# Kernel optimization log

Measured on AMD Instinct MI355X. Metric: run time of the kernel, lower is better.

## Reference

```python
import jax, jax.numpy as jnp
import numpy as np

HEAD_NUM = 12
HEAD_SIZE = 64
INPUT_DIM = 768
BATCH = 2
SEQ = 2048
NEG = 1e12


def setup_inputs() -> dict:
    key = jax.random.key(0)
    k1, k2, k3 = jax.random.split(key, 3)
    x = jax.random.normal(k1, (BATCH, SEQ, INPUT_DIM), dtype=jnp.float32)
    W = jax.random.normal(k2, (INPUT_DIM, HEAD_NUM * HEAD_SIZE * 2), dtype=jnp.float32) * 0.02
    b = jax.random.normal(k3, (HEAD_NUM * HEAD_SIZE * 2,), dtype=jnp.float32) * 0.02
    mask = jnp.ones((BATCH, SEQ), dtype=jnp.int32)
    return {"x": x, "W": W, "b": b, "mask": mask}


def _rope_tables(n, d, dtype):
    # SinusoidalPositionEmbedding(head_size, 'zero'): pos[..., 0::2]=sin, 1::2=cos
    pos = jnp.arange(n, dtype=dtype)
    freqs = jnp.power(10000.0, -2.0 * jnp.arange(d // 2, dtype=dtype) / d)
    ang = pos[:, None] * freqs[None, :]  # [n, d/2]
    # K.repeat_elements(pos[..., 1::2], 2, -1) -> each cos value repeated twice
    cos_pos = jnp.repeat(jnp.cos(ang), 2, axis=-1)  # [n, d]
    sin_pos = jnp.repeat(jnp.sin(ang), 2, axis=-1)  # [n, d]
    return cos_pos[None, :, None, :], sin_pos[None, :, None, :]  # [1,n,1,d]


def _rotate_half(t):
    # stack([-t[...,1::2], t[...,::2]], -1).reshape(t.shape)
    t2 = jnp.stack([-t[..., 1::2], t[..., 0::2]], axis=-1)
    return t2.reshape(t.shape)


def reference(x, W, b, mask):
    bsz, n, _ = x.shape
    proj = (x @ W + b).reshape(bsz, n, HEAD_NUM, 2 * HEAD_SIZE)  # [b,n,h,2d]
    qw, kw = proj[..., :HEAD_SIZE], proj[..., HEAD_SIZE:]
    cos_pos, sin_pos = _rope_tables(n, HEAD_SIZE, x.dtype)
    qw = qw * cos_pos + _rotate_half(qw) * sin_pos
    kw = kw * cos_pos + _rotate_half(kw) * sin_pos
    logits = jnp.einsum('bmhd,bnhd->bhmn', qw, kw)  # [b,h,m,n]
    m = mask.astype(logits.dtype)
    logits = logits - (1.0 - m[:, None, :, None]) * NEG  # mask query axis (dim 2)
    logits = logits - (1.0 - m[:, None, None, :]) * NEG  # mask key axis (dim 3)
    tri = jnp.triu(jnp.ones((n, n), dtype=logits.dtype))  # band_part(0,-1): keep m<=n
    logits = logits - (1.0 - tri) * NEG
    return logits / (HEAD_SIZE ** 0.5)
```

## Files before the change

### kernel.cpp

```cpp
#include <hip/hip_runtime.h>

#define SEQ    2048
#define IND    768
#define NPROJ  1536
#define BHN    24
#define NEGV   1000000000000.0f

typedef __attribute__((ext_vector_type(4))) float f32x4;
typedef __attribute__((ext_vector_type(8))) short s16x8;
typedef __attribute__((ext_vector_type(8))) unsigned short u16x8;
typedef __attribute__((ext_vector_type(4))) unsigned short u16x4;

__device__ __forceinline__ unsigned short f2bf(float f) {
  unsigned int u = __builtin_bit_cast(unsigned int, f);
  u += 0x7fffu + ((u >> 16) & 1u);
  return (unsigned short)(u >> 16);
}

__device__ __forceinline__ void nt_store4(float* p, f32x4 v) {
  __builtin_nontemporal_store(v, (f32x4*)p);
}

__device__ __forceinline__ void barrier_lgkm() {
  asm volatile("s_waitcnt lgkmcnt(0)" ::: "memory");
  __builtin_amdgcn_s_barrier();
}

#define GLOAD_LDS16(g, l)                                              \
  __builtin_amdgcn_global_load_lds(                                    \
      (const __attribute__((address_space(1))) void*)(g),              \
      (__attribute__((address_space(3))) void*)(l), 16, 0, 0)

__device__ __forceinline__ void stage128x64(const unsigned short* __restrict__ src,
                                            size_t stride, int4* lds, int tid) {
  const int w = tid >> 6, l = tid & 63;
#pragma unroll
  for (int i = 0; i < 4; ++i) {
    int gb = w * 256 + i * 64;
    int G = gb + l;
    int row = G >> 3, g = G & 7;
    int cb = g ^ (row & 7);
    GLOAD_LDS16(src + (size_t)row * stride + cb * 8, lds + gb);
  }
}

__device__ __forceinline__ void fill_tile(int fid, const int* __restrict__ mask,
                                          float* __restrict__ out, int tid) {
  int bh = fid / 120;
  int t = fid - bh * 120;
  int mt = 1;
  while (t >= mt) { t -= mt; ++mt; }
  int nt = t;
  int b = bh / 12;
  int m0 = mt * 128, n0 = nt * 128;
  const float scale = 0.125f;
#pragma unroll
  for (int it = 0; it < 16; ++it) {
    int id = it * 256 + tid;
    int row = id >> 5, c4 = id & 31;
    int gm = m0 + row;
    float rm = (float)mask[b * SEQ + gm];
    int gn0 = n0 + c4 * 4;
    f32x4 v;
#pragma unroll
    for (int q = 0; q < 4; ++q) {
      float cm = (float)mask[b * SEQ + gn0 + q];
      v[q] = -(NEGV * ((1.f - rm) + (1.f - cm) + 1.f)) * scale;
    }
    nt_store4(out + ((size_t)bh * SEQ + gm) * SEQ + gn0, v);
  }
}

__global__ __launch_bounds__(256) void k_prep(const float* __restrict__ x,
                                              const float* __restrict__ W,
                                              unsigned short* __restrict__ xb,
                                              unsigned short* __restrict__ Wt,
                                              float* __restrict__ cosT,
                                              float* __restrict__ sinT,
                                              const int* __restrict__ mask,
                                              float* __restrict__ out) {
  __shared__ float Ws[64][65];
  const int bid = blockIdx.x;
  const int tid = threadIdx.x;

  if (bid < 1536) {
    int i = (bid * 256 + tid) * 8;
    float4 a = *(const float4*)(x + i);
    float4 b = *(const float4*)(x + i + 4);
    u16x8 o;
    o[0] = f2bf(a.x); o[1] = f2bf(a.y); o[2] = f2bf(a.z); o[3] = f2bf(a.w);
    o[4] = f2bf(b.x); o[5] = f2bf(b.y); o[6] = f2bf(b.z); o[7] = f2bf(b.w);
    *(u16x8*)(xb + i) = o;
  } else if (bid < 1824) {
    int tb = bid - 1536;
    int nt = tb % 24, kt = tb / 24;
    int n0 = nt * 64, k0 = kt * 64;
    int cr = tid >> 4;
    int cc = (tid & 15) * 4;
#pragma unroll
    for (int it = 0; it < 4; ++it) {
      int kr = it * 16 + cr;
      float4 v = *(const float4*)(W + (size_t)(k0 + kr) * NPROJ + n0 + cc);
      Ws[kr][cc + 0] = v.x; Ws[kr][cc + 1] = v.y;
      Ws[kr][cc + 2] = v.z; Ws[kr][cc + 3] = v.w;
    }
    __syncthreads();
#pragma unroll
    for (int it = 0; it < 4; ++it) {
      int nl = it * 16 + cr;
      u16x4 o;
#pragma unroll
      for (int q = 0; q < 4; ++q) o[q] = f2bf(Ws[cc + q][nl]);
      *(u16x4*)(Wt + (size_t)(n0 + nl) * IND + k0 + cc) = o;
    }
  } else if (bid < 2080) {
    int i = (bid - 1824) * 256 + tid;
    int s = i >> 5, f = i & 31;
    float freq = exp2f(-(float)f * (13.287712379549449f / 32.0f));
    float ang = (float)s * freq;
    float sv, cv;
    sincosf(ang, &sv, &cv);
    cosT[i] = cv; sinT[i] = sv;
  } else {
    fill_tile(bid - 2080, mask, out, tid);
  }
}

__global__ __launch_bounds__(256, 2) void k_projfill(const unsigned short* __restrict__ xb,
                                                     const unsigned short* __restrict__ Wt,
                                                     const float* __restrict__ bias,
                                                     unsigned short* __restrict__ Qb,
                                                     unsigned short* __restrict__ Kb,
                                                     const float* __restrict__ cosT,
                                                     const float* __restrict__ sinT,
                                                     const int* __restrict__ mask,
                                                     float* __restrict__ out) {
  __shared__ int4 smem2[4096];
  const int tid = threadIdx.x;

  if (blockIdx.x >= 384) {
    fill_tile(512 + (int)blockIdx.x - 384, mask, out, tid);
    return;
  }

  int4* As4 = smem2;
  int4* Bs4 = smem2 + 2048;
  const int bidl = blockIdx.x;
  const int bid = (bidl & 7) * 48 + (bidl >> 3);
  const int nt = bid % 12, mt = bid / 12;
  const int m0 = mt * 128, n0 = nt * 128;
  const int wid = tid >> 6, lane = tid & 63;
  const int wr = wid >> 1, wc = wid & 1;
  const int lr = lane & 15, kg = lane >> 4;

  f32x4 acc[4][4] = {};

  const unsigned short* Abase = xb + (size_t)m0 * IND;
  const unsigned short* Bbase = Wt + (size_t)n0 * IND;

  stage128x64(Abase, IND, As4, tid);
  stage128x64(Bbase, IND, Bs4, tid);
  __syncthreads();

  for (int kt = 0; kt < 12; ++kt) {
    int cur = kt & 1;
    if (kt < 11) {
      stage128x64(Abase + (kt + 1) * 64, IND, As4 + (cur ^ 1) * 1024, tid);
      stage128x64(Bbase + (kt + 1) * 64, IND, Bs4 + (cur ^ 1) * 1024, tid);
    }
    const int4* Ac = As4 + cur * 1024;
    const int4* Bc = Bs4 + cur * 1024;
#pragma unroll
    for (int kk = 0; kk < 2; ++kk) {
      s16x8 af[4], bfr[4];
#pragma unroll
      for (int i = 0; i < 4; ++i) {
        int r = wr * 64 + i * 16 + lr;
        af[i] = *(const s16x8*)&Ac[r * 8 + ((kk * 4 + kg) ^ (r & 7))];
      }
#pragma unroll
      for (int j = 0; j < 4; ++j) {
        int r = wc * 64 + j * 16 + lr;
        bfr[j] = *(const s16x8*)&Bc[r * 8 + ((kk * 4 + kg) ^ (r & 7))];
      }
#pragma unroll
      for (int i = 0; i < 4; ++i)
#pragma unroll
        for (int j = 0; j < 4; ++j)
          acc[i][j] = __builtin_amdgcn_mfma_f32_16x16x32_bf16(af[i], bfr[j], acc[i][j], 0, 0, 0);
    }
    __syncthreads();
  }

  unsigned short* Cs = (unsigned short*)As4;
#pragma unroll
  for (int i = 0; i < 4; ++i) {
#pragma unroll
    for (int j = 0; j < 4; ++j) {
      int colr = wc * 64 + j * 16 + lr;
      int col = n0 + colr;
      float bcol = bias[col];
      int d = col & 63;
#pragma unroll
      for (int r = 0; r < 4; ++r) {
        int rowr = wr * 64 + i * 16 + kg * 4 + r;
        int s = (m0 + rowr) & (SEQ - 1);
        float v = acc[i][j][r] + bcol;
        float p = __shfl_xor(v, 1);
        int ti = s * 32 + (d >> 1);
        float cv = cosT[ti], sv = sinT[ti];
        float o = (col & 1) ? (v * cv + p * sv) : (v * cv - p * sv);
        int gs = (colr >> 3) ^ (rowr & 15);
        Cs[rowr * 128 + gs * 8 + (colr & 7)] = f2bf(o);
      }
    }
  }
  barrier_lgkm();
#pragma unroll
  for (int it = 0; it < 8; ++it) {
    int id = it * 256 + tid;
    int rowr = id >> 4, g = id & 15;
    int gs = g ^ (rowr & 15);
    u16x8 v = *(const u16x8*)&Cs[rowr * 128 + gs * 8];
    int m = m0 + rowr;
    int s = m & (SEQ - 1), bb = m >> 11;
    int colg = n0 + g * 8;
    int h = colg >> 7;
    int d0 = colg & 63;
    unsigned short* dst = ((colg & 64) == 0) ? Qb : Kb;
    *(u16x8*)(dst + ((size_t)(bb * 12 + h) * SEQ + s) * 64 + d0) = v;
  }
}

__global__ __launch_bounds__(256, 4) void k_attn(const unsigned short* __restrict__ Qb,
                                                 const unsigned short* __restrict__ Kb,
                                                 const int* __restrict__ mask,
                                                 float* __restrict__ out) {
  __shared__ int4 smem[2048];
  int4* Qs4 = smem;
  int4* Ks4 = smem + 1024;

  const int b0 = blockIdx.x;
  const int lin = (b0 & 7) * 408 + (b0 >> 3);
  int bh = lin / 136;
  int t = lin - bh * 136;
  int mt = 0;
  while (t >= 16 - mt) { t -= 16 - mt; ++mt; }
  const int nt = mt + t;
  const int b = bh / 12;
  const int tid = threadIdx.x;
  const int m0 = mt * 128, n0 = nt * 128;
  const float scale = 0.125f;

  const int wid = tid >> 6, lane = tid & 63;
  const int wr = wid >> 1, wc = wid & 1;
  const int lr = lane & 15, kg = lane >> 4;

  stage128x64(Qb + ((size_t)bh * SEQ + m0) * 64, 64, Qs4, tid);
  stage128x64(Kb + ((size_t)bh * SEQ + n0) * 64, 64, Ks4, tid);
  __syncthreads();

  f32x4 acc[4][4] = {};
#pragma unroll
  for (int kk = 0; kk < 2; ++kk) {
    s16x8 af[4], bfr[4];
#pragma unroll
    for (int i = 0; i < 4; ++i) {
      int r = wr * 64 + i * 16 + lr;
      af[i] = *(const s16x8*)&Qs4[r * 8 + ((kk * 4 + kg) ^ (r & 7))];
    }
#pragma unroll
    for (int j = 0; j < 4; ++j) {
      int r = wc * 64 + j * 16 + lr;
      bfr[j] = *(const s16x8*)&Ks4[r * 8 + ((kk * 4 + kg) ^ (r & 7))];
    }
#pragma unroll
    for (int i = 0; i < 4; ++i)
#pragma unroll
      for (int j = 0; j < 4; ++j)
        acc[i][j] = __builtin_amdgcn_mfma_f32_16x16x32_bf16(af[i], bfr[j], acc[i][j], 0, 0, 0);
  }

  barrier_lgkm();
  float* Cs = (float*)smem;

#pragma unroll
  for (int c = 0; c < 2; ++c) {
    if (wr == c) {
#pragma unroll
      for (int i = 0; i < 4; ++i)
#pragma unroll
        for (int j = 0; j < 4; ++j) {
          int col = wc * 64 + j * 16 + lr;
          int g = col >> 2;
#pragma unroll
          for (int r = 0; r < 4; ++r) {
            int rl = i * 16 + kg * 4 + r;
            int gs = g ^ (rl & 7);
            Cs[rl * 128 + gs * 4 + (col & 3)] = acc[i][j][r];
          }
        }
    }
    barrier_lgkm();
#pragma unroll
    for (int it = 0; it < 8; ++it) {
      int id = it * 256 + tid;
      int rl = id >> 5, g = id & 31;
      int gs = g ^ (rl & 7);
      f32x4 v = *(const f32x4*)&Cs[rl * 128 + gs * 4];
      int gm = m0 + c * 64 + rl;
      int gn0 = n0 + g * 4;
      float rmv = (float)mask[b * SEQ + gm];
      int4 cm = *(const int4*)&mask[b * SEQ + gn0];
      f32x4 o;
#pragma unroll
      for (int q = 0; q < 4; ++q) {
        int gn = gn0 + q;
        float cmv = (float)((const int*)&cm)[q];
        float pen = (1.f - rmv) + (1.f - cmv) + ((gn < gm) ? 1.f : 0.f);
        o[q] = (v[q] - NEGV * pen) * scale;
      }
      nt_store4(out + ((size_t)bh * SEQ + gm) * SEQ + gn0, o);
    }
    if (c == 0) barrier_lgkm();
  }
}

extern "C" void kernel_launch(void* const* d_in, const int* in_sizes, int n_in,
                              void* d_out, int out_size, void* d_ws, size_t ws_size,
                              hipStream_t stream) {
  const float* x    = (const float*)d_in[0];
  const float* W    = (const float*)d_in[1];
  const float* bias = (const float*)d_in[2];
  const int*   mask = (const int*)d_in[3];
  float* out = (float*)d_out;

  char* ws = (char*)d_ws;
  unsigned short* xb = (unsigned short*)(ws);
  unsigned short* Wt = (unsigned short*)(ws + 6291456);
  unsigned short* Qb = (unsigned short*)(ws + 6291456 + 2359296);
  unsigned short* Kb = (unsigned short*)(ws + 6291456 + 2359296 + 6291456);
  float* cosT = (float*)(ws + 6291456 + 2359296 + 6291456 + 6291456);
  float* sinT = (float*)(ws + 6291456 + 2359296 + 6291456 + 6291456 + 262144);

  k_prep<<<2592, 256, 0, stream>>>(x, W, xb, Wt, cosT, sinT, mask, out);
  k_projfill<<<2752, 256, 0, stream>>>(xb, Wt, bias, Qb, Kb, cosT, sinT, mask, out);
  k_attn<<<3264, 256, 0, stream>>>(Qb, Kb, mask, out);
}
```

Baseline: 94.97 us.

## Swap MFMA operand roles to store epilogues directly from registers, drop LDS staging

Both the projection GEMM and the attention-logits kernel swap the A/B operands of the MFMA so each lane's accumulator holds four consecutive output columns. The epilogues then apply bias, RoPE, masking and scaling in registers and write 8-byte (bf16) or 16-byte (fp32) vectors straight to global memory. This removes the LDS round trip and its barriers. In exchange, each wavefront's stores cover 16 rows with 64-byte segments per row instead of full contiguous rows, which may reduce write coalescing on the large fp32 output.

```diff
diff --git a/kernel.cpp b/kernel.cpp
--- a/kernel.cpp
+++ b/kernel.cpp
@@ -19,11 +19,6 @@
 
 __device__ __forceinline__ void nt_store4(float* p, f32x4 v) {
   __builtin_nontemporal_store(v, (f32x4*)p);
-}
-
-__device__ __forceinline__ void barrier_lgkm() {
-  asm volatile("s_waitcnt lgkmcnt(0)" ::: "memory");
-  __builtin_amdgcn_s_barrier();
 }
 
 #define GLOAD_LDS16(g, l)                                              \
@@ -175,13 +170,13 @@
       s16x8 af[4], bfr[4];
 #pragma unroll
       for (int i = 0; i < 4; ++i) {
-        int r = wr * 64 + i * 16 + lr;
-        af[i] = *(const s16x8*)&Ac[r * 8 + ((kk * 4 + kg) ^ (r & 7))];
+        int r = wc * 64 + i * 16 + lr;
+        af[i] = *(const s16x8*)&Bc[r * 8 + ((kk * 4 + kg) ^ (r & 7))];
       }
 #pragma unroll
       for (int j = 0; j < 4; ++j) {
-        int r = wc * 64 + j * 16 + lr;
-        bfr[j] = *(const s16x8*)&Bc[r * 8 + ((kk * 4 + kg) ^ (r & 7))];
+        int r = wr * 64 + j * 16 + lr;
+        bfr[j] = *(const s16x8*)&Ac[r * 8 + ((kk * 4 + kg) ^ (r & 7))];
       }
 #pragma unroll
       for (int i = 0; i < 4; ++i)
@@ -192,43 +187,28 @@
     __syncthreads();
   }
 
-  unsigned short* Cs = (unsigned short*)As4;
-#pragma unroll
-  for (int i = 0; i < 4; ++i) {
-#pragma unroll
-    for (int j = 0; j < 4; ++j) {
-      int colr = wc * 64 + j * 16 + lr;
-      int col = n0 + colr;
-      float bcol = bias[col];
-      int d = col & 63;
-#pragma unroll
-      for (int r = 0; r < 4; ++r) {
-        int rowr = wr * 64 + i * 16 + kg * 4 + r;
-        int s = (m0 + rowr) & (SEQ - 1);
-        float v = acc[i][j][r] + bcol;
-        float p = __shfl_xor(v, 1);
-        int ti = s * 32 + (d >> 1);
-        float cv = cosT[ti], sv = sinT[ti];
-        float o = (col & 1) ? (v * cv + p * sv) : (v * cv - p * sv);
-        int gs = (colr >> 3) ^ (rowr & 15);
-        Cs[rowr * 128 + gs * 8 + (colr & 7)] = f2bf(o);
-      }
-    }
-  }
-  barrier_lgkm();
-#pragma unroll
-  for (int it = 0; it < 8; ++it) {
-    int id = it * 256 + tid;
-    int rowr = id >> 4, g = id & 15;
-    int gs = g ^ (rowr & 15);
-    u16x8 v = *(const u16x8*)&Cs[rowr * 128 + gs * 8];
-    int m = m0 + rowr;
-    int s = m & (SEQ - 1), bb = m >> 11;
-    int colg = n0 + g * 8;
-    int h = colg >> 7;
-    int d0 = colg & 63;
-    unsigned short* dst = ((colg & 64) == 0) ? Qb : Kb;
-    *(u16x8*)(dst + ((size_t)(bb * 12 + h) * SEQ + s) * 64 + d0) = v;
+#pragma unroll
+  for (int j = 0; j < 4; ++j) {
+    int gm = m0 + wr * 64 + j * 16 + lr;
+    int s = gm & (SEQ - 1), bb = gm >> 11;
+#pragma unroll
+    for (int i = 0; i < 4; ++i) {
+      int col0 = n0 + wc * 64 + i * 16 + kg * 4;
+      int d0 = col0 & 63;
+      int h = col0 >> 7;
+      f32x4 bi = *(const f32x4*)&bias[col0];
+      int fi = s * 32 + (d0 >> 1);
+      float c0 = cosT[fi],     s0 = sinT[fi];
+      float c1 = cosT[fi + 1], s1 = sinT[fi + 1];
+      f32x4 v = acc[i][j] + bi;
+      u16x4 o;
+      o[0] = f2bf(v[0] * c0 - v[1] * s0);
+      o[1] = f2bf(v[1] * c0 + v[0] * s0);
+      o[2] = f2bf(v[2] * c1 - v[3] * s1);
+      o[3] = f2bf(v[3] * c1 + v[2] * s1);
+      unsigned short* dst = ((col0 & 64) == 0) ? Qb : Kb;
+      *(u16x4*)(dst + ((size_t)(bb * 12 + h) * SEQ + s) * 64 + d0) = o;
+    }
   }
 }
 
@@ -266,13 +246,13 @@
     s16x8 af[4], bfr[4];
 #pragma unroll
     for (int i = 0; i < 4; ++i) {
-      int r = wr * 64 + i * 16 + lr;
-      af[i] = *(const s16x8*)&Qs4[r * 8 + ((kk * 4 + kg) ^ (r & 7))];
+      int r = wc * 64 + i * 16 + lr;
+      af[i] = *(const s16x8*)&Ks4[r * 8 + ((kk * 4 + kg) ^ (r & 7))];
     }
 #pragma unroll
     for (int j = 0; j < 4; ++j) {
-      int r = wc * 64 + j * 16 + lr;
-      bfr[j] = *(const s16x8*)&Ks4[r * 8 + ((kk * 4 + kg) ^ (r & 7))];
+      int r = wr * 64 + j * 16 + lr;
+      bfr[j] = *(const s16x8*)&Qs4[r * 8 + ((kk * 4 + kg) ^ (r & 7))];
     }
 #pragma unroll
     for (int i = 0; i < 4; ++i)
@@ -281,37 +261,16 @@
         acc[i][j] = __builtin_amdgcn_mfma_f32_16x16x32_bf16(af[i], bfr[j], acc[i][j], 0, 0, 0);
   }
 
-  barrier_lgkm();
-  float* Cs = (float*)smem;
-
-#pragma unroll
-  for (int c = 0; c < 2; ++c) {
-    if (wr == c) {
-#pragma unroll
-      for (int i = 0; i < 4; ++i)
-#pragma unroll
-        for (int j = 0; j < 4; ++j) {
-          int col = wc * 64 + j * 16 + lr;
-          int g = col >> 2;
-#pragma unroll
-          for (int r = 0; r < 4; ++r) {
-            int rl = i * 16 + kg * 4 + r;
-            int gs = g ^ (rl & 7);
-            Cs[rl * 128 + gs * 4 + (col & 3)] = acc[i][j][r];
-          }
-        }
-    }
-    barrier_lgkm();
-#pragma unroll
-    for (int it = 0; it < 8; ++it) {
-      int id = it * 256 + tid;
-      int rl = id >> 5, g = id & 31;
-      int gs = g ^ (rl & 7);
-      f32x4 v = *(const f32x4*)&Cs[rl * 128 + gs * 4];
-      int gm = m0 + c * 64 + rl;
-      int gn0 = n0 + g * 4;
-      float rmv = (float)mask[b * SEQ + gm];
+#pragma unroll
+  for (int j = 0; j < 4; ++j) {
+    int gm = m0 + wr * 64 + j * 16 + lr;
+    float rmv = (float)mask[b * SEQ + gm];
+    float* orow = out + ((size_t)bh * SEQ + gm) * SEQ;
+#pragma unroll
+    for (int i = 0; i < 4; ++i) {
+      int gn0 = n0 + wc * 64 + i * 16 + kg * 4;
       int4 cm = *(const int4*)&mask[b * SEQ + gn0];
+      f32x4 v = acc[i][j];
       f32x4 o;
 #pragma unroll
       for (int q = 0; q < 4; ++q) {
@@ -320,9 +279,8 @@
         float pen = (1.f - rmv) + (1.f - cmv) + ((gn < gm) ? 1.f : 0.f);
         o[q] = (v[q] - NEGV * pen) * scale;
       }
-      nt_store4(out + ((size_t)bh * SEQ + gm) * SEQ + gn0, o);
-    }
-    if (c == 0) barrier_lgkm();
+      nt_store4(orow + gn0, o);
+    }
   }
 }
 
```

Result: slower. 118.7 us (+24.9%).
